# Kernel tuning notes

Measured on AMD Instinct MI355X. Metric: run time of the kernel, lower is better.

## Reference

```python
import jax, jax.numpy as jnp
import numpy as np

BS, C, H, W = 128, 256, 9, 9
D = 9                      # spectral window size
PS = 15                    # padsize
PAD_SPACE = PS - H         # 6
PAD1 = D // 2              # 4 (spectral pad)
START = PAD_SPACE // 2     # 3 (output crop offset)
SPE_HEAD = 25
SHARE_HEAD = 9
SIDE = 5                   # spe_head_Sidelength
BN_EPS = 1e-5


def setup_inputs() -> dict:
    key = jax.random.key(0)
    ks = jax.random.split(key, 12)
    s = 0.1
    return {
        "x": jax.random.normal(ks[0], (BS, C, H, W), jnp.float32),
        "wk": jax.random.normal(ks[1], (H * W, 1, D), jnp.float32) * s,   # depthwise conv1d over spectral axis
        "bk": jax.random.normal(ks[2], (H * W,), jnp.float32) * s,
        "w1": jax.random.normal(ks[3], (SPE_HEAD, SHARE_HEAD, 2 * SHARE_HEAD), jnp.float32) * s,  # grouped 1x1, no bias
        "bn_gamma": jnp.ones((SPE_HEAD * SHARE_HEAD,), jnp.float32),
        "bn_beta": jnp.zeros((SPE_HEAD * SHARE_HEAD,), jnp.float32),
        "bn_mean": jax.random.normal(ks[4], (SPE_HEAD * SHARE_HEAD,), jnp.float32) * s,
        "bn_var": jax.random.uniform(ks[5], (SPE_HEAD * SHARE_HEAD,), jnp.float32, 0.5, 1.5),
        "w2": jax.random.normal(ks[6], (SPE_HEAD, D, SHARE_HEAD), jnp.float32) * s,  # grouped 1x1 -> spe_head*d
        "b2": jax.random.normal(ks[7], (SPE_HEAD * D,), jnp.float32) * s,
        "wv": jax.random.normal(ks[8], (C, 1, 3, 3), jnp.float32) * s,   # depthwise 3x3
        "bv": jax.random.normal(ks[9], (C,), jnp.float32) * s,
    }


def _unfold_k3_d5(t, bs, c):
    # torch nn.Unfold(kernel=3, dilation=5) on a 15x15 map -> 5x5 output positions.
    # row = kh*5 + oh, col = kw*5 + ow, so a plain (3,5,3,5) reshape gives the taps.
    t = t.reshape(bs, c, 3, SIDE, 3, SIDE)              # (bs,c,kh,oh,kw,ow)
    t = t.transpose(0, 1, 2, 4, 3, 5)                   # (bs,c,kh,kw,oh,ow)
    t = t.reshape(bs, c * SHARE_HEAD, SPE_HEAD)          # (bs, c*9, 25) torch unfold layout
    return t.transpose(0, 2, 1)                          # (bs, 25, c*9)


def reference(x, wk, bk, w1, bn_gamma, bn_beta, bn_mean, bn_var, w2, b2, wv, bv):
    bs, c, h, w = x.shape
    # --- key: depthwise conv1d along spectral (channel) axis, one filter per pixel ---
    k = x.reshape(bs, c, h * w).transpose(0, 2, 1)       # (bs, 81, c)
    k1 = jax.lax.conv_general_dilated(
        k, wk, (1,), [(PAD1, PAD1)],
        dimension_numbers=("NCH", "OIH", "NCH"), feature_group_count=h * w,
    ) + bk[None, :, None]                                # (bs, 81, c)
    k1 = k1.transpose(0, 2, 1).reshape(bs, c, h, w)

    # --- pad right/bottom and unfold q, k ---
    k1_pad = jnp.pad(k1, ((0, 0), (0, 0), (0, PAD_SPACE), (0, PAD_SPACE)))  # (bs,c,15,15)
    q_pad = jnp.pad(x, ((0, 0), (0, 0), (0, PAD_SPACE), (0, PAD_SPACE)))
    key_u = _unfold_k3_d5(k1_pad, bs, c)                 # (bs,25,9c)
    q_u = _unfold_k3_d5(q_pad, bs, c)

    # stack + reshape exactly as torch (row-major): (bs,25,2,9c) -> (bs,450,c)
    key_q = jnp.stack((q_u, key_u), axis=2).reshape(bs, 2 * SPE_HEAD * SHARE_HEAD, c)

    # --- attention_embed: grouped 1x1 conv -> BN(eval) -> ReLU -> grouped 1x1 conv ---
    a = jnp.einsum("goi,bgic->bgoc", w1, key_q.reshape(bs, SPE_HEAD, 2 * SHARE_HEAD, c))
    a = a.reshape(bs, SPE_HEAD * SHARE_HEAD, c)          # (bs,225,c)
    inv_std = bn_gamma / jnp.sqrt(bn_var + BN_EPS)
    a = (a - bn_mean[None, :, None]) * inv_std[None, :, None] + bn_beta[None, :, None]
    a = jax.nn.relu(a)
    a = jnp.einsum("goi,bgic->bgoc", w2, a.reshape(bs, SPE_HEAD, SHARE_HEAD, c))
    a = a.reshape(bs, SPE_HEAD * D, c) + b2[None, :, None]  # (bs,225,c)

    # --- build per-pixel spectral kernels: tile, rearrange to 15x15, softmax over d ---
    att = jnp.tile(a.reshape(bs, SPE_HEAD, D, c), (1, SHARE_HEAD, 1, 1))  # (bs,225,9,c)
    att = att.transpose(0, 3, 1, 2)                      # (bs,c,225,d)
    att = att.reshape(bs, c, 3, 3, SIDE, SIDE, D)
    att = att.transpose(0, 1, 2, 4, 3, 5, 6)             # swap dims 3,4 as torch .transpose(3,4)
    att = att.reshape(bs, c, PS, PS, D)
    att = jax.nn.softmax(att, axis=-1)
    att = att.transpose(0, 1, 4, 2, 3)                   # (bs,c,d,15,15)

    # --- value: depthwise 3x3 conv, pad left/top + spectral, sliding window over channels ---
    v = jax.lax.conv_general_dilated(
        x, wv, (1, 1), [(1, 1), (1, 1)],
        dimension_numbers=("NCHW", "OIHW", "NCHW"), feature_group_count=c,
    ) + bv[None, :, None, None]                          # (bs,c,9,9)
    pv = jnp.pad(v, ((0, 0), (PAD1, PAD1), (PAD_SPACE, 0), (PAD_SPACE, 0)))  # (bs,c+8,15,15)
    v_unf = jnp.stack([pv[:, t:t + c] for t in range(D)], axis=2)            # (bs,c,d,15,15)

    out = jnp.sum(v_unf * att, axis=2) + k1_pad          # (bs,c,15,15)
    return out[:, :, START:h + START, START:w + START]    # (bs,c,9,9)
```

## Files before the change

kernel.cpp:

```cpp
#include <hip/hip_runtime.h>

#define C 256
#define HW 81
#define PITCH 266
#define PITCHD 133
#define ZROW 81

__device__ __forceinline__ float lo_f(unsigned int d) {
  union { unsigned int i; float f; } c; c.i = d << 16; return c.f;
}
__device__ __forceinline__ float hi_f(unsigned int d) {
  union { unsigned int i; float f; } c; c.i = d & 0xffff0000u; return c.f;
}
__device__ __forceinline__ float bf2f(unsigned short u) {
  union { unsigned int i; float f; } c; c.i = ((unsigned int)u) << 16; return c.f;
}
__device__ __forceinline__ unsigned short f2bf(float f) {
  union { float f; unsigned int i; } c; c.f = f;
  return (unsigned short)((c.i + 0x7fffu + ((c.i >> 16) & 1u)) >> 16);
}
__device__ __forceinline__ unsigned int pack2(float a, float b) {
  return (unsigned int)f2bf(a) | ((unsigned int)f2bf(b) << 16);
}

__global__ __launch_bounds__(1024) void semca_fused(
    const float* __restrict__ x, const float* __restrict__ wk,
    const float* __restrict__ bk, const float* __restrict__ w1,
    const float* __restrict__ gamma, const float* __restrict__ beta,
    const float* __restrict__ mean, const float* __restrict__ var,
    const float* __restrict__ w2, const float* __restrict__ b2,
    const float* __restrict__ wv, const float* __restrict__ bv,
    float* __restrict__ out) {
  __shared__ unsigned short xT[82 * PITCH];
  __shared__ unsigned short k1T[82 * PITCH];
  __shared__ unsigned short vT[18 * PITCH];
  __shared__ float wvs[C * 9];
  __shared__ unsigned short pixtab[228];
  __shared__ float2 bnf[225];

  const int blk = blockIdx.x;
  const int b = (blk & 7) * 16 + ((blk >> 3) & 15);
  const int s = blk >> 7;
  const int tid = threadIdx.x;
  const float* xb = x + (size_t)b * (C * HW);

  unsigned int* xTd = (unsigned int*)xT;
  unsigned int* k1Td = (unsigned int*)k1T;
  unsigned int* vTd = (unsigned int*)vT;

  {
    auto stage = [&](int f) {
      int chp = f / HW;
      int p = f - chp * HW;
      xTd[PITCHD * p + 2 + chp] =
          pack2(xb[(2 * chp) * HW + p], xb[(2 * chp + 1) * HW + p]);
    };
#pragma unroll
    for (int rep = 0; rep < 10; ++rep) stage(tid + rep * 1024);
    if (tid < 128) stage(10240 + tid);
  }
  for (int t = tid; t < 810; t += 1024) {
    int p = t / 10, k2 = t - (t / 10) * 10;
    xT[p * PITCH + ((k2 < 4) ? k2 : (256 + k2))] = 0;
  }
  if (tid < PITCHD) {
    xTd[PITCHD * ZROW + tid] = 0;
    k1Td[PITCHD * ZROW + tid] = 0;
  }
  for (int t = tid; t < C * 9; t += 1024) wvs[t] = wv[t];
  for (int t = tid; t < 225; t += 1024) {
    int g = t / 9, tap = t - (t / 9) * 9;
    int kh = tap / 3, kw = tap - kh * 3;
    int h = kh * 5 + g / 5, w = kw * 5 + (g - (g / 5) * 5);
    pixtab[t] = (h < 9 && w < 9) ? (unsigned short)(h * 9 + w)
                                 : (unsigned short)ZROW;
    float inv = gamma[t] * rsqrtf(var[t] + 1e-5f);
    bnf[t] = make_float2(inv, beta[t] - mean[t] * inv);
  }
  __syncthreads();

  {
    auto k1fn = [&](int f) {
      int p = __builtin_amdgcn_readfirstlane(f >> 7);
      int chp = f & 127;
      const unsigned int* wrow = xTd + PITCHD * p;
      unsigned int d0 = wrow[chp], d1 = wrow[chp + 1], d2 = wrow[chp + 2],
                   d3 = wrow[chp + 3], d4 = wrow[chp + 4];
      float e[10] = {lo_f(d0), hi_f(d0), lo_f(d1), hi_f(d1), lo_f(d2),
                     hi_f(d2), lo_f(d3), hi_f(d3), lo_f(d4), hi_f(d4)};
      const float* wkp = wk + p * 9;
      float bkp = bk[p];
      float a_e = bkp, a_o = bkp;
#pragma unroll
      for (int j = 0; j < 9; ++j) {
        float wj = wkp[j];
        a_e = fmaf(wj, e[j], a_e);
        a_o = fmaf(wj, e[j + 1], a_o);
      }
      k1Td[PITCHD * p + 2 + chp] = pack2(a_e, a_o);
    };
#pragma unroll
    for (int rep = 0; rep < 10; ++rep) k1fn(tid + rep * 1024);
    if (tid < 128) k1fn(10240 + tid);
  }

  {
    auto vfn = [&](int f) {
      int e = __builtin_amdgcn_readfirstlane(f >> 7);
      int chp = f & 127;
      int r0 = e / 6;
      int i = s * 3 + r0;
      int j = e - r0 * 6;
      float a_e = bv[2 * chp], a_o = bv[2 * chp + 1];
      const float* wv_e = wvs + (2 * chp) * 9;
      const float* wv_o = wv_e + 9;
#pragma unroll
      for (int di = 0; di < 3; ++di) {
        int ii = i + di - 1;
        if (ii < 0) continue;
#pragma unroll
        for (int dj = 0; dj < 3; ++dj) {
          int jj = j + dj - 1;
          if (jj < 0) continue;
          unsigned int d = xTd[PITCHD * (ii * 9 + jj) + 2 + chp];
          int t = di * 3 + dj;
          a_e = fmaf(lo_f(d), wv_e[t], a_e);
          a_o = fmaf(hi_f(d), wv_o[t], a_o);
        }
      }
      vTd[PITCHD * e + 2 + chp] = pack2(a_e, a_o);
    };
#pragma unroll
    for (int rep = 0; rep < 2; ++rep) vfn(tid + rep * 1024);
    if (tid < 256) vfn(2048 + tid);
  }
  if (tid < 180) {
    int e = tid / 10, k2 = tid - (tid / 10) * 10;
    vT[e * PITCH + ((k2 < 4) ? k2 : (256 + k2))] = 0;
  }
  __syncthreads();

  const int s4 = tid >> 8;
  const int ch = tid & 255;
  const int ci0 = ch / 9;
  const int tap0 = ch - ci0 * 9;
  float* outb = out + ((size_t)b * C + ch) * HW;

#define PV_STORE(OH, OW)                                                   \
  do {                                                                     \
    int e_ = gh_i * 6 + ((OW)-3);                                          \
    const unsigned short* vrow_ = vT + e_ * PITCH;                         \
    float acc_ = 0.f;                                                      \
    _Pragma("unroll") for (int d_ = 0; d_ < 9; ++d_) acc_ =                \
        fmaf(a2[d_], bf2f(vrow_[ch + d_]), acc_);                          \
    acc_ *= inv_s;                                                         \
    if ((OH) < 6 && (OW) < 6)                                              \
      acc_ += bf2f(k1T[(((OH) + 3) * 9 + ((OW) + 3)) * PITCH + 4 + ch]);   \
    if (valid_inst) outb[(OH)*9 + (OW)] = acc_;                            \
  } while (0)

#pragma unroll
  for (int k = 0; k < 4; ++k) {
    int idx = s4 * 4 + k;
    const bool valid_inst = (idx < 15);
    if (!valid_inst) idx = 14;
    int gh_i = idx / 5, gw_i = idx - (idx / 5) * 5;
    int oh = (s ? 6 : 3) + gh_i;
    int gh = s ? ((gh_i + 4) % 5) : (gh_i + 1);
    int g9 = __builtin_amdgcn_readfirstlane((gh * 5 + gw_i) * 9);

    float kq[18];
    int ci = ci0, tap = tap0;
#pragma unroll
    for (int q = 0; q < 9; ++q) {
      int off = (int)pixtab[g9 + tap] * PITCH + 4 + ci;
      kq[q] = bf2f(xT[off]);
      kq[9 + q] = bf2f(k1T[off]);
      tap += 4;
      ci += 28;
      if (tap >= 9) { tap -= 9; ci += 1; }
    }

    float r[9];
#pragma unroll
    for (int o = 0; o < 9; ++o) {
      int m = g9 + o;
      const float* w1m = w1 + m * 18;
      float a = 0.f;
#pragma unroll
      for (int i2 = 0; i2 < 18; ++i2) a = fmaf(w1m[i2], kq[i2], a);
      float2 bn = bnf[m];
      a = fmaf(a, bn.x, bn.y);
      r[o] = fmaxf(a, 0.f);
    }

    float a2[9], mx = -1e30f;
#pragma unroll
    for (int d = 0; d < 9; ++d) {
      int m = g9 + d;
      const float* w2m = w2 + m * 9;
      float a = b2[m];
#pragma unroll
      for (int o = 0; o < 9; ++o) a = fmaf(w2m[o], r[o], a);
      a2[d] = a;
      mx = fmaxf(mx, a);
    }
    float ssum = 0.f;
#pragma unroll
    for (int d = 0; d < 9; ++d) {
      a2[d] = __expf(a2[d] - mx);
      ssum += a2[d];
    }
    float inv_s = 1.f / ssum;

    int ow0 = (gw_i == 0) ? 7 : (gw_i + 2);
    PV_STORE(oh, ow0);
    if (gw_i == 1) PV_STORE(oh, 8);
  }
#undef PV_STORE

  if (s == 0) {
    if (s4 < 3) {
      int oh = s4;
#pragma unroll
      for (int ow = 0; ow < 9; ++ow) {
        float v2 = 0.f;
        if (ow < 6)
          v2 = bf2f(k1T[((oh + 3) * 9 + (ow + 3)) * PITCH + 4 + ch]);
        outb[oh * 9 + ow] = v2;
      }
    } else {
#pragma unroll
      for (int r0 = 0; r0 < 3; ++r0) {
        int oh = 3 + r0;
#pragma unroll
        for (int ow = 0; ow < 3; ++ow)
          outb[oh * 9 + ow] =
              bf2f(k1T[((oh + 3) * 9 + (ow + 3)) * PITCH + 4 + ch]);
      }
    }
  } else if (s4 < 3) {
    int oh = 6 + s4;
    outb[oh * 9 + 0] = 0.f;
    outb[oh * 9 + 1] = 0.f;
    outb[oh * 9 + 2] = 0.f;
  }
}

extern "C" void kernel_launch(void* const* d_in, const int* in_sizes, int n_in,
                              void* d_out, int out_size, void* d_ws, size_t ws_size,
                              hipStream_t stream) {
  const float* x     = (const float*)d_in[0];
  const float* wk    = (const float*)d_in[1];
  const float* bk    = (const float*)d_in[2];
  const float* w1    = (const float*)d_in[3];
  const float* gamma = (const float*)d_in[4];
  const float* beta  = (const float*)d_in[5];
  const float* mean  = (const float*)d_in[6];
  const float* var   = (const float*)d_in[7];
  const float* w2    = (const float*)d_in[8];
  const float* b2    = (const float*)d_in[9];
  const float* wv    = (const float*)d_in[10];
  const float* bv    = (const float*)d_in[11];
  float* out = (float*)d_out;

  hipLaunchKernelGGL(semca_fused, dim3(256), dim3(1024), 0, stream,
                     x, wk, bk, w1, gamma, beta, mean, var, w2, b2, wv, bv, out);
}
```

Measured before the change: 27.78 us.

## Hoist depthwise weights into registers, precompute tap offsets, raise wave priority in compute

Removes the shared-memory staging of the 3x3 value weights and instead loads each thread's per-channel weights and biases into registers once, before the barrier. The pixel table now stores pre-multiplied row offsets, and the per-thread tap/channel index sequence is computed once outside the loop instead of per iteration. The compute-heavy MLP/softmax section is wrapped in s_setprio to favour those waves, and the softmax normalisation uses a hardware reciprocal. This saves shared-memory traffic and integer ALU work at the cost of more registers per thread, which may hurt occupancy at 1024 threads per block.

```diff
diff --git a/kernel.cpp b/kernel.cpp
--- a/kernel.cpp
+++ b/kernel.cpp
@@ -34,7 +34,6 @@
   __shared__ unsigned short xT[82 * PITCH];
   __shared__ unsigned short k1T[82 * PITCH];
   __shared__ unsigned short vT[18 * PITCH];
-  __shared__ float wvs[C * 9];
   __shared__ unsigned short pixtab[228];
   __shared__ float2 bnf[225];
 
@@ -67,16 +66,25 @@
     xTd[PITCHD * ZROW + tid] = 0;
     k1Td[PITCHD * ZROW + tid] = 0;
   }
-  for (int t = tid; t < C * 9; t += 1024) wvs[t] = wv[t];
   for (int t = tid; t < 225; t += 1024) {
     int g = t / 9, tap = t - (t / 9) * 9;
     int kh = tap / 3, kw = tap - kh * 3;
     int h = kh * 5 + g / 5, w = kw * 5 + (g - (g / 5) * 5);
-    pixtab[t] = (h < 9 && w < 9) ? (unsigned short)(h * 9 + w)
-                                 : (unsigned short)ZROW;
+    pixtab[t] = (h < 9 && w < 9) ? (unsigned short)((h * 9 + w) * PITCH)
+                                 : (unsigned short)(ZROW * PITCH);
     float inv = gamma[t] * rsqrtf(var[t] + 1e-5f);
     bnf[t] = make_float2(inv, beta[t] - mean[t] * inv);
   }
+
+  const int chv = tid & 127;
+  float wv_e[9], wv_o[9];
+#pragma unroll
+  for (int t = 0; t < 9; ++t) {
+    wv_e[t] = wv[(2 * chv) * 9 + t];
+    wv_o[t] = wv[(2 * chv + 1) * 9 + t];
+  }
+  const float bv_e = bv[2 * chv], bv_o = bv[2 * chv + 1];
+
   __syncthreads();
 
   {
@@ -107,13 +115,10 @@
   {
     auto vfn = [&](int f) {
       int e = __builtin_amdgcn_readfirstlane(f >> 7);
-      int chp = f & 127;
       int r0 = e / 6;
       int i = s * 3 + r0;
       int j = e - r0 * 6;
-      float a_e = bv[2 * chp], a_o = bv[2 * chp + 1];
-      const float* wv_e = wvs + (2 * chp) * 9;
-      const float* wv_o = wv_e + 9;
+      float a_e = bv_e, a_o = bv_o;
 #pragma unroll
       for (int di = 0; di < 3; ++di) {
         int ii = i + di - 1;
@@ -122,13 +127,13 @@
         for (int dj = 0; dj < 3; ++dj) {
           int jj = j + dj - 1;
           if (jj < 0) continue;
-          unsigned int d = xTd[PITCHD * (ii * 9 + jj) + 2 + chp];
+          unsigned int d = xTd[PITCHD * (ii * 9 + jj) + 2 + chv];
           int t = di * 3 + dj;
           a_e = fmaf(lo_f(d), wv_e[t], a_e);
           a_o = fmaf(hi_f(d), wv_o[t], a_o);
         }
       }
-      vTd[PITCHD * e + 2 + chp] = pack2(a_e, a_o);
+      vTd[PITCHD * e + 2 + chv] = pack2(a_e, a_o);
     };
 #pragma unroll
     for (int rep = 0; rep < 2; ++rep) vfn(tid + rep * 1024);
@@ -145,6 +150,19 @@
   const int ci0 = ch / 9;
   const int tap0 = ch - ci0 * 9;
   float* outb = out + ((size_t)b * C + ch) * HW;
+
+  int tq[9], cq[9];
+  {
+    int ci = ci0, tap = tap0;
+#pragma unroll
+    for (int q = 0; q < 9; ++q) {
+      tq[q] = tap;
+      cq[q] = 4 + ci;
+      tap += 4;
+      ci += 28;
+      if (tap >= 9) { tap -= 9; ci += 1; }
+    }
+  }
 
 #define PV_STORE(OH, OW)                                                   \
   do {                                                                     \
@@ -170,17 +188,14 @@
     int g9 = __builtin_amdgcn_readfirstlane((gh * 5 + gw_i) * 9);
 
     float kq[18];
-    int ci = ci0, tap = tap0;
 #pragma unroll
     for (int q = 0; q < 9; ++q) {
-      int off = (int)pixtab[g9 + tap] * PITCH + 4 + ci;
+      int off = (int)pixtab[g9 + tq[q]] + cq[q];
       kq[q] = bf2f(xT[off]);
       kq[9 + q] = bf2f(k1T[off]);
-      tap += 4;
-      ci += 28;
-      if (tap >= 9) { tap -= 9; ci += 1; }
-    }
-
+    }
+
+    __builtin_amdgcn_s_setprio(1);
     float r[9];
 #pragma unroll
     for (int o = 0; o < 9; ++o) {
@@ -211,7 +226,8 @@
       a2[d] = __expf(a2[d] - mx);
       ssum += a2[d];
     }
-    float inv_s = 1.f / ssum;
+    float inv_s = __builtin_amdgcn_rcpf(ssum);
+    __builtin_amdgcn_s_setprio(0);
 
     int ow0 = (gw_i == 0) ? 7 : (gw_i + 2);
     PV_STORE(oh, ow0);
```

After: 27.96 us. Within noise of the previous version (+0.6%).
